# Kernel optimization log

Measured on AMD Instinct MI355X. Metric: run time of the kernel, lower is better.

## Reference

```python
import jax, jax.numpy as jnp
import numpy as np

B_PAIR = 8      # batch_size (identities)
NUM_POS = 4     # images per identity
TEMP = 50.0     # softmax temperature
DIM = 2048
H, W = 24, 12
HALF = B_PAIR * NUM_POS  # 32 samples per modality


def _rand_pairs(rng):
    # mirrors CMAlign._random_pairs
    pos = np.concatenate([rng.permutation(NUM_POS) + NUM_POS * i for i in range(B_PAIR)])
    neg = []
    for i in range(B_PAIR):
        others = np.array([j for j in range(B_PAIR) if j != i])
        bidx = rng.choice(others, NUM_POS, replace=False)
        nidx = rng.permutation(NUM_POS)
        neg.append(bidx * NUM_POS + nidx)
    return pos.astype(np.int32), np.concatenate(neg).astype(np.int32)


def setup_inputs() -> dict:
    key = jax.random.key(0)
    ks = jax.random.split(key, 8)
    feat_v = jax.random.normal(ks[0], (HALF, DIM, H, W), jnp.float32)
    feat_t = jax.random.normal(ks[1], (HALF, DIM, H, W), jnp.float32)
    uncertain_v = jax.random.normal(ks[2], (HALF, 1, H, W), jnp.float32)
    uncertain_t = jax.random.normal(ks[3], (HALF, 1, H, W), jnp.float32)
    q_w = jax.random.normal(ks[4], (DIM // 4, DIM, 3, 3), jnp.float32) * 0.02
    q_b = jnp.zeros((DIM // 4,), jnp.float32)
    k_w = jax.random.normal(ks[5], (DIM // 4, DIM, 3, 3), jnp.float32) * 0.02
    k_b = jnp.zeros((DIM // 4,), jnp.float32)
    rng = np.random.RandomState(0)
    pos_v, neg_v = _rand_pairs(rng)
    pos_t, neg_t = _rand_pairs(rng)
    # visible queries target thermal half (offset), thermal queries target visible half
    pos_idx = jnp.asarray(np.concatenate([pos_v + HALF, pos_t]), jnp.int32)
    neg_idx = jnp.asarray(np.concatenate([neg_v + HALF, neg_t]), jnp.int32)
    return dict(feat_v=feat_v, feat_t=feat_t, uncertain_v=uncertain_v,
                uncertain_t=uncertain_t, q_w=q_w, q_b=q_b, k_w=k_w, k_b=k_b,
                pos_idx=pos_idx, neg_idx=neg_idx)


def _conv3x3(x, w, b):
    y = jax.lax.conv_general_dilated(x, w, window_strides=(1, 1),
                                     padding=((1, 1), (1, 1)),
                                     dimension_numbers=('NCHW', 'OIHW', 'NCHW'))
    return y + b[None, :, None, None]


def _l2n(x, axis):
    # torch F.normalize: x / max(||x||, 1e-12)
    n = jnp.sqrt(jnp.sum(x * x, axis=axis, keepdims=True))
    return x / jnp.maximum(n, 1e-12)


def _cmalign(feat_v, feat_t, q_w, q_b, k_w, k_b, pos_idx, neg_idx):
    feat = jnp.concatenate([feat_v, feat_t], axis=0)  # [B,C,h,w]
    B, C, h, w = feat.shape
    HW = h * w

    # compute_mask (detached): per-sample min-max normalized channel L2 norm
    norms = jnp.sqrt(jnp.sum(feat * feat, axis=1)).reshape(B, HW)
    norms = norms - jnp.min(norms, axis=-1, keepdims=True)
    norms = norms / (jnp.max(norms, axis=-1, keepdims=True) + 1e-12)
    mask = jax.lax.stop_gradient(norms.reshape(B, 1, h, w))

    fq = _conv3x3(feat, q_w, q_b).reshape(B, C // 4, HW)  # query proj shared

    def matching_pr(target):
        fk = _conv3x3(target, k_w, k_b).reshape(B, C // 4, HW)
        sim = jnp.einsum('bcq,bck->bqk', _l2n(fq, 1), _l2n(fk, 1))
        # max-subtract + exp + sum == stable softmax with temperature
        return jax.nn.softmax(TEMP * sim, axis=-1)

    def warp_recon(pr, target):
        warp = jnp.einsum('bqk,bck->bcq', pr, target.reshape(B, C, HW)).reshape(B, C, h, w)
        return mask * warp + (1.0 - mask) * feat

    # positive branch
    tgt_pos = feat[pos_idx]
    pr_pos = matching_pr(tgt_pos)
    mq = mask.reshape(B, HW, 1)
    mk = mask[pos_idx].reshape(B, HW, 1)
    comask = (mq * jnp.einsum('bqk,bko->bqo', pr_pos, mk)).reshape(B, HW)
    comask = comask - jnp.min(comask, axis=-1, keepdims=True)
    comask = comask / (jnp.max(comask, axis=-1, keepdims=True) + 1e-12)
    comask = jax.lax.stop_gradient(comask.reshape(B, h, w))
    feat_recon_pos = warp_recon(pr_pos, tgt_pos)

    # negative branch
    tgt_neg = feat[neg_idx]
    feat_recon_neg = warp_recon(matching_pr(tgt_neg), tgt_neg)

    # triplet margin loss (p=2, margin=0.3, eps=1e-6), distance over channel dim
    d_ap = jnp.sqrt(jnp.sum((feat - feat_recon_pos + 1e-6) ** 2, axis=1))  # [B,h,w]
    d_an = jnp.sqrt(jnp.sum((feat - feat_recon_neg + 1e-6) ** 2, axis=1))
    trip = jnp.maximum(d_ap - d_an + 0.3, 0.0)
    loss = jnp.mean(comask * trip)
    return feat_recon_pos, loss


def reference(feat_v, feat_t, uncertain_v, uncertain_t, q_w, q_b, k_w, k_b, pos_idx, neg_idx):
    # uncertain_v/uncertain_t are concatenated but unused in CMAlign.forward (faithful)
    del uncertain_v, uncertain_t
    return _cmalign(feat_v, feat_t, q_w, q_b, k_w, k_b, pos_idx, neg_idx)
```

## Files before the change

### kernel.cpp

```cpp
#include <hip/hip_runtime.h>
#include <cstdint>
#include <cstddef>


namespace {
constexpr int kB    = 64;
constexpr int kHalf = 32;
constexpr int kC    = 2048;
constexpr int kCQ   = 512;
constexpr int kH    = 24;
constexpr int kW    = 12;
constexpr int kHW   = 288;
constexpr float kTemp = 50.0f;
constexpr int kXPlane = 366;
}

typedef __attribute__((ext_vector_type(8))) __bf16 bf16x8;
typedef __attribute__((ext_vector_type(4))) float f32x4;
typedef __attribute__((ext_vector_type(8))) unsigned short ushort8;

__device__ __forceinline__ const float* feat_base(const float* fv, const float* ft, int b) {
  return (b < kHalf) ? (fv + (size_t)b * kC * kHW)
                     : (ft + (size_t)(b - kHalf) * kC * kHW);
}

__device__ __forceinline__ unsigned short f2bf(float f) {
  union { float f; unsigned u; } c; c.f = f;
  unsigned u = c.u;
  unsigned r = (u + 0x7FFFu + ((u >> 16) & 1u)) >> 16;
  return (unsigned short)r;
}

__device__ __forceinline__ float bf2f(unsigned short h) {
  union { unsigned u; float f; } c; c.u = ((unsigned)h) << 16;
  return c.f;
}

__device__ __forceinline__ void gload_lds16(const void* g, void* l) {
  __builtin_amdgcn_global_load_lds(
      (const __attribute__((address_space(1))) unsigned int*)g,
      (__attribute__((address_space(3))) unsigned int*)l, 16, 0, 0);
}

__global__ void zero_kernel(float* __restrict__ p, int n) {
  int i = blockIdx.x * 256 + threadIdx.x;
  if (i < n) p[i] = 0.f;
}

__global__ __launch_bounds__(256) void prep_w_kernel(const float* __restrict__ qw,
                                                     const float* __restrict__ kw,
                                                     unsigned short* __restrict__ wtq,
                                                     unsigned short* __restrict__ wtk) {
  int oc = blockIdx.x;
  int z  = blockIdx.y;
  const float* w = (z ? kw : qw) + (size_t)oc * (kC * 9);
  unsigned short* wt = z ? wtk : wtq;
  __shared__ unsigned short lw[kC * 9];
  int t = threadIdx.x;
#pragma unroll
  for (int it = 0; it < 18; ++it) {
    int i4 = (it * 256 + t) * 4;
    float4 v = *(const float4*)(w + i4);
    lw[i4 + 0] = f2bf(v.x);
    lw[i4 + 1] = f2bf(v.y);
    lw[i4 + 2] = f2bf(v.z);
    lw[i4 + 3] = f2bf(v.w);
  }
  __syncthreads();
  for (int item = t; item < 9 * 256; item += 256) {
    int tap = item >> 8;
    int icb = item & 255;
    ushort8 pk;
#pragma unroll
    for (int j = 0; j < 8; ++j) pk[j] = lw[(icb * 8 + j) * 9 + tap];
    size_t dst16 = (((size_t)(icb >> 2) * 9 + tap) * 32 + (oc >> 4)) * 64
                   + (oc & 15) + (icb & 3) * 16;
    *(ushort8*)(wt + dst16 * 8) = pk;
  }
}

__global__ __launch_bounds__(512, 1) void conv_fused_kernel(const unsigned short* __restrict__ wtq,
                                                            const unsigned short* __restrict__ wtk,
                                                            const float* __restrict__ qb,
                                                            const float* __restrict__ kb,
                                                            const float* __restrict__ fv,
                                                            const float* __restrict__ ft,
                                                            unsigned short* __restrict__ fqT,
                                                            unsigned short* __restrict__ fkT,
                                                            float* __restrict__ qss,
                                                            float* __restrict__ kss) {
  __shared__ unsigned short Wbuf[2 * 6 * 4096];
  __shared__ unsigned short Xs[4 * kXPlane * 8];
  int t    = threadIdx.x;
  int lane = t & 63;
  int wid  = t >> 6;
  int l15  = lane & 15, kg = lane >> 4;
  int wm   = wid & 1, wn = wid >> 1;
  int n    = blockIdx.x;
  int xcd  = n & 7;
  int oc0  = (xcd >> 1) * 128;
  int b    = ((xcd & 1) << 5) + (n >> 3);
  int f0   = oc0 >> 4;
  const float* fb = feat_base(fv, ft, b);
  const char* wtqB = (const char*)wtq;
  const char* wtkB = (const char*)wtk;

  int  xoff[3];
  bool xvalid[3], xhas[3];
#pragma unroll
  for (int i = 0; i < 3; ++i) {
    int item = i * 512 + t;
    xhas[i] = item < 4 * kXPlane;
    int xkg = item / kXPlane;
    int hp  = item - xkg * kXPlane;
    int hy = hp / 14, hx = hp - hy * 14;
    int y = hy - 1, x = hx - 1;
    bool v = xhas[i] && hp < 364 && (y >= 0 && y < kH && x >= 0 && x < kW);
    xvalid[i] = v;
    xoff[i] = v ? (xkg * 8) * kHW + y * kW + x : 0;
  }

  int aAddr[4];
#pragma unroll
  for (int fm = 0; fm < 4; ++fm)
    aAddr[fm] = (((wm * 4 + fm) * 64) + lane) * 16;
  int nfn = (wn < 2) ? 5 : 4;
  int fnb = (wn < 2) ? wn * 5 : 10 + (wn - 2) * 4;
  int bAddr[5];
#pragma unroll
  for (int fi = 0; fi < 5; ++fi) {
    int p = (fnb + fi) * 16 + l15;
    if (p > 287) p = 287;
    int y = p / kW, x = p - y * kW;
    bAddr[fi] = kg * (kXPlane * 16) + ((y + 1) * 14 + (x + 1)) * 16;
  }

  f32x4 acc[2][4][5];
#pragma unroll
  for (int cv = 0; cv < 2; ++cv)
#pragma unroll
    for (int fm = 0; fm < 4; ++fm)
#pragma unroll
      for (int fi = 0; fi < 5; ++fi) acc[cv][fm][fi] = (f32x4){0.f, 0.f, 0.f, 0.f};

  char* WsB = (char*)Wbuf;
  char* XsB = (char*)Xs;
  int wavebase = t & ~63;

#pragma unroll
  for (int i = 0; i < 3; ++i) {
    if (xhas[i] && !xvalid[i]) {
      ushort8 pk;
#pragma unroll
      for (int j = 0; j < 8; ++j) pk[j] = 0;
      *(ushort8*)(XsB + (size_t)(i * 512 + t) * 16) = pk;
    }
  }
#pragma unroll
  for (int r = 0; r < 3; ++r) {
    size_t g16 = ((size_t)r * 32 + f0 + wid) * 64 + lane;
    gload_lds16(wtqB + g16 * 16, WsB + (size_t)(r * 2 + 0) * 8192 + wavebase * 16);
    gload_lds16(wtkB + g16 * 16, WsB + (size_t)(r * 2 + 1) * 8192 + wavebase * 16);
  }

  int buf = 0;
#pragma unroll 1
  for (int chunk = 0; chunk < 64; ++chunk) {
    int ic0 = chunk * 32;
    {
      float xv[3][8];
#pragma unroll
      for (int i = 0; i < 3; ++i)
        if (xvalid[i]) {
          const float* s = fb + (size_t)ic0 * kHW + xoff[i];
#pragma unroll
          for (int j = 0; j < 8; ++j) xv[i][j] = s[(size_t)j * kHW];
        }
#pragma unroll
      for (int i = 0; i < 3; ++i) {
        if (!xvalid[i]) continue;
        ushort8 pk;
#pragma unroll
        for (int j = 0; j < 8; ++j) pk[j] = f2bf(xv[i][j]);
        *(ushort8*)(XsB + (size_t)(i * 512 + t) * 16) = pk;
      }
    }
    __syncthreads();

#pragma unroll 1
    for (int g = 0; g < 3; ++g) {
      bool hn = (g < 2) || (chunk < 63);
      if (hn) {
        int nchunk = (g < 2) ? chunk : chunk + 1;
        int ng     = (g < 2) ? g + 1 : 0;
#pragma unroll
        for (int r = 0; r < 3; ++r) {
          size_t g16 = ((size_t)(nchunk * 9 + ng * 3 + r) * 32 + f0 + wid) * 64 + lane;
          gload_lds16(wtqB + g16 * 16,
                      WsB + (size_t)((buf ^ 1) * 6 + r * 2 + 0) * 8192 + wavebase * 16);
          gload_lds16(wtkB + g16 * 16,
                      WsB + (size_t)((buf ^ 1) * 6 + r * 2 + 1) * 8192 + wavebase * 16);
        }
      }
#pragma unroll
      for (int r = 0; r < 3; ++r) {
        int tap = g * 3 + r;
        int d16 = ((tap / 3 - 1) * 14 + (tap % 3 - 1)) * 16;
        bf16x8 af[2][4];
#pragma unroll
        for (int cv = 0; cv < 2; ++cv)
#pragma unroll
          for (int fm = 0; fm < 4; ++fm)
            af[cv][fm] = *(const bf16x8*)(WsB + (size_t)(buf * 6 + r * 2 + cv) * 8192 + aAddr[fm]);
#pragma unroll
        for (int fi = 0; fi < 5; ++fi) {
          if (fi >= nfn) continue;
          bf16x8 bb = *(const bf16x8*)(XsB + bAddr[fi] + d16);
#pragma unroll
          for (int cv = 0; cv < 2; ++cv)
#pragma unroll
            for (int fm = 0; fm < 4; ++fm)
              acc[cv][fm][fi] =
                  __builtin_amdgcn_mfma_f32_16x16x32_bf16(af[cv][fm], bb, acc[cv][fm][fi], 0, 0, 0);
        }
      }
      __syncthreads();
      buf ^= 1;
    }
  }

  unsigned short* Ep = Wbuf;
#pragma unroll
  for (int cv = 0; cv < 2; ++cv) {
    const float* bias = cv ? kb : qb;
    float* ssq = cv ? kss : qss;
#pragma unroll
    for (int fi = 0; fi < 5; ++fi) {
      if (fi >= nfn) continue;
      int p = (fnb + fi) * 16 + l15;
      float ps = 0.f;
#pragma unroll
      for (int fm = 0; fm < 4; ++fm)
#pragma unroll
        for (int reg = 0; reg < 4; ++reg) {
          int ocl = wm * 64 + fm * 16 + kg * 4 + reg;
          float v = acc[cv][fm][fi][reg] + bias[oc0 + ocl];
          ps = fmaf(v, v, ps);
          Ep[p * 136 + ocl] = f2bf(v);
        }
      ps += __shfl_xor(ps, 16);
      ps += __shfl_xor(ps, 32);
      if (kg == 0) atomicAdd(ssq + b * kHW + p, ps);
    }
    __syncthreads();
    unsigned short* dstT = (cv ? fkT : fqT) + (size_t)b * kHW * kCQ + oc0;
#pragma unroll
    for (int it = 0; it < 9; ++it) {
      int item = it * 512 + t;
      int p = item >> 4, j = item & 15;
      *(ushort8*)(dstT + (size_t)p * kCQ + j * 8) =
          *(const ushort8*)(Ep + p * 136 + j * 8);
    }
    __syncthreads();
  }
}

__global__ __launch_bounds__(512) void warp_mfma_kernel(const float* __restrict__ fv,
                                                        const float* __restrict__ ft,
                                                        const unsigned short* __restrict__ prb0,
                                                        const unsigned short* __restrict__ prb1,
                                                        const float* __restrict__ maskp,
                                                        const int* __restrict__ pos_idx,
                                                        const int* __restrict__ neg_idx,
                                                        float* __restrict__ outp,
                                                        float* __restrict__ dap,
                                                        float* __restrict__ dan) {
  __shared__ unsigned short AsHi[128 * 32];
  __shared__ unsigned short AsLo[128 * 32];
  __shared__ unsigned short Bs[288 * 32];
  int t    = threadIdx.x;
  int lane = t & 63;
  int wid  = t >> 6;
  int l15  = lane & 15, kg = lane >> 4;
  int wm   = wid >> 1, wn = wid & 1;
  int c0   = blockIdx.x * 128;
  int b    = blockIdx.y;
  int z    = blockIdx.z;
  int write_out = (z == 0);
  const unsigned short* prb = z ? prb1 : prb0;
  float* dsq = z ? dan : dap;
  int tb   = (z ? neg_idx : pos_idx)[b];
  const float* tgt = feat_base(fv, ft, tb);
  const float* fb  = feat_base(fv, ft, b);

  int ar = t >> 2, as = t & 3;
  int aslot = as ^ ((ar ^ (ar >> 2)) & 3);
  unsigned short* aDstHi = AsHi + ar * 32 + aslot * 8;
  unsigned short* aDstLo = AsLo + ar * 32 + aslot * 8;

  int aIdx[2];
#pragma unroll
  for (int fm = 0; fm < 2; ++fm) {
    int r = wm * 32 + fm * 16 + l15;
    aIdx[fm] = r * 32 + (kg ^ ((r ^ (r >> 2)) & 3)) * 8;
  }
  int bIdx[9];
#pragma unroll
  for (int fn = 0; fn < 9; ++fn) {
    int q = wn * 144 + fn * 16 + l15;
    bIdx[fn] = q * 32 + (kg ^ ((q ^ (q >> 2)) & 3)) * 8;
  }

  f32x4 acc[2][9];
#pragma unroll
  for (int fm = 0; fm < 2; ++fm)
#pragma unroll
    for (int fn = 0; fn < 9; ++fn) acc[fm][fn] = (f32x4){0.f, 0.f, 0.f, 0.f};

#pragma unroll 1
  for (int chunk = 0; chunk < 9; ++chunk) {
    int k0 = chunk * 32;
    __syncthreads();
    {
      const float* s = tgt + (size_t)(c0 + ar) * kHW + k0 + as * 8;
      float4 v0 = *(const float4*)(s);
      float4 v1 = *(const float4*)(s + 4);
      float xs[8] = {v0.x, v0.y, v0.z, v0.w, v1.x, v1.y, v1.z, v1.w};
      ushort8 hi, lo;
#pragma unroll
      for (int j = 0; j < 8; ++j) {
        unsigned short h = f2bf(xs[j]);
        hi[j] = h;
        lo[j] = f2bf(xs[j] - bf2f(h));
      }
      *(ushort8*)aDstHi = hi;
      *(ushort8*)aDstLo = lo;
    }
#pragma unroll
    for (int i = 0; i < 3; ++i) {
      int item = i * 512 + t;
      if (item < 1152) {
        int q = item >> 2, s = item & 3;
        ushort8 v = *(const ushort8*)(prb + ((size_t)b * kHW + q) * kHW + k0 + s * 8);
        *(ushort8*)(Bs + q * 32 + (s ^ ((q ^ (q >> 2)) & 3)) * 8) = v;
      }
    }
    __syncthreads();
    bf16x8 ah0 = *(const bf16x8*)(AsHi + aIdx[0]);
    bf16x8 al0 = *(const bf16x8*)(AsLo + aIdx[0]);
    bf16x8 ah1 = *(const bf16x8*)(AsHi + aIdx[1]);
    bf16x8 al1 = *(const bf16x8*)(AsLo + aIdx[1]);
#pragma unroll
    for (int fn = 0; fn < 9; ++fn) {
      bf16x8 bb = *(const bf16x8*)(Bs + bIdx[fn]);
      acc[0][fn] = __builtin_amdgcn_mfma_f32_16x16x32_bf16(ah0, bb, acc[0][fn], 0, 0, 0);
      acc[0][fn] = __builtin_amdgcn_mfma_f32_16x16x32_bf16(al0, bb, acc[0][fn], 0, 0, 0);
      acc[1][fn] = __builtin_amdgcn_mfma_f32_16x16x32_bf16(ah1, bb, acc[1][fn], 0, 0, 0);
      acc[1][fn] = __builtin_amdgcn_mfma_f32_16x16x32_bf16(al1, bb, acc[1][fn], 0, 0, 0);
    }
  }

#pragma unroll
  for (int fn = 0; fn < 9; ++fn) {
    int q = wn * 144 + fn * 16 + l15;
    float mj = maskp[b * kHW + q];
    float psum = 0.f;
#pragma unroll
    for (int fm = 0; fm < 2; ++fm) {
#pragma unroll
      for (int reg = 0; reg < 4; ++reg) {
        int c = c0 + wm * 32 + fm * 16 + kg * 4 + reg;
        float fvv = fb[(size_t)c * kHW + q];
        float Wv  = acc[fm][fn][reg];
        float d   = mj * (fvv - Wv) + 1e-6f;
        psum      = fmaf(d, d, psum);
        if (write_out)
          outp[((size_t)b * kC + c) * kHW + q] = mj * Wv + (1.f - mj) * fvv;
      }
    }
    psum += __shfl_xor(psum, 16);
    psum += __shfl_xor(psum, 32);
    if (lane < 16) atomicAdd(&dsq[b * kHW + q], psum);
  }
}

__global__ __launch_bounds__(320) void mask_part_kernel(const float* __restrict__ fv,
                                                        const float* __restrict__ ft,
                                                        float* __restrict__ part) {
  int b = blockIdx.x;
  int s = blockIdx.y;
  int t = threadIdx.x;
  if (t >= kHW) return;
  const float* fb = feat_base(fv, ft, b) + (size_t)(s * 512) * kHW;
  float sum = 0.f;
  for (int c = 0; c < 512; ++c) { float v = fb[(size_t)c * kHW + t]; sum += v * v; }
  part[((size_t)b * 4 + s) * kHW + t] = sum;
}

__global__ __launch_bounds__(320) void mask_fin_kernel(const float* __restrict__ part,
                                                       float* __restrict__ mask) {
  int b = blockIdx.x;
  int t = threadIdx.x;
  float n = 0.f;
  if (t < kHW) {
    const float* pb = part + (size_t)b * 4 * kHW;
    n = sqrtf(pb[t] + pb[kHW + t] + pb[2 * kHW + t] + pb[3 * kHW + t]);
  }
  __shared__ float sh[320];
  sh[t] = (t < kHW) ? n : 3.4e38f;
  __syncthreads();
  float mn;
  {
    float m = 3.4e38f;
    if (t < 64) {
      for (int i = t; i < 320; i += 64) m = fminf(m, sh[i]);
      for (int off = 32; off; off >>= 1) m = fminf(m, __shfl_xor(m, off));
    }
    __syncthreads();
    if (t == 0) sh[0] = m;
    __syncthreads();
    mn = sh[0];
    __syncthreads();
  }
  sh[t] = (t < kHW) ? n : -3.4e38f;
  __syncthreads();
  float mx;
  {
    float m = -3.4e38f;
    if (t < 64) {
      for (int i = t; i < 320; i += 64) m = fmaxf(m, sh[i]);
      for (int off = 32; off; off >>= 1) m = fmaxf(m, __shfl_xor(m, off));
    }
    __syncthreads();
    if (t == 0) sh[0] = m;
    __syncthreads();
    mx = sh[0];
  }
  if (t < kHW) mask[b * kHW + t] = (n - mn) / ((mx - mn) + 1e-12f);
}

__global__ __launch_bounds__(512, 1) void sim_mfma_kernel(const unsigned short* __restrict__ fqT,
                                                          const unsigned short* __restrict__ fkT,
                                                          const float* __restrict__ qss,
                                                          const float* __restrict__ kss,
                                                          const int* __restrict__ pos_idx,
                                                          const int* __restrict__ neg_idx,
                                                          unsigned short* __restrict__ prb0,
                                                          unsigned short* __restrict__ prb1) {
  __shared__ float Sbuf[96 * 289];
  unsigned short* As = (unsigned short*)Sbuf;
  unsigned short* Bs = (unsigned short*)((char*)Sbuf + 6144);
  float (*S)[289] = (float(*)[289])Sbuf;
  int t    = threadIdx.x;
  int lane = t & 63;
  int wid  = t >> 6;
  int l15  = lane & 15, kg = lane >> 4;
  int wm   = wid & 1, wn = wid >> 1;
  int q0   = blockIdx.x * 96;
  int b    = blockIdx.y;
  int z    = blockIdx.z;
  int tb   = (z ? neg_idx : pos_idx)[b];
  unsigned short* prb = z ? prb1 : prb0;
  const unsigned short* fqb = fqT + ((size_t)b * kHW + q0) * kCQ;
  const unsigned short* fkb = fkT + (size_t)tb * kHW * kCQ;

  int aIdx[3];
#pragma unroll
  for (int fm = 0; fm < 3; ++fm) {
    int r = wm * 48 + fm * 16 + l15;
    aIdx[fm] = r * 32 + (kg ^ ((r ^ (r >> 2)) & 3)) * 8;
  }
  int nfn = (wn < 2) ? 5 : 4;
  int fnb = (wn < 2) ? wn * 5 : 10 + (wn - 2) * 4;
  int bIdx[5];
#pragma unroll
  for (int fi = 0; fi < 5; ++fi) {
    int kr = (fnb + fi) * 16 + l15;
    if (kr > 287) kr = 287;
    bIdx[fi] = kr * 32 + (kg ^ ((kr ^ (kr >> 2)) & 3)) * 8;
  }

  f32x4 acc[3][5];
#pragma unroll
  for (int fm = 0; fm < 3; ++fm)
#pragma unroll
    for (int fi = 0; fi < 5; ++fi) acc[fm][fi] = (f32x4){0.f, 0.f, 0.f, 0.f};

#pragma unroll 1
  for (int chunk = 0; chunk < 16; ++chunk) {
    int c0 = chunk * 32;
    __syncthreads();
    if (t < 384) {
      int ar = t >> 2, as = t & 3;
      ushort8 v = *(const ushort8*)(fqb + (size_t)ar * kCQ + c0 + as * 8);
      int slot = as ^ ((ar ^ (ar >> 2)) & 3);
      *(ushort8*)(As + ar * 32 + slot * 8) = v;
    }
#pragma unroll
    for (int i = 0; i < 3; ++i) {
      int item = i * 512 + t;
      if (item < 1152) {
        int kr = item >> 2, ks = item & 3;
        ushort8 v = *(const ushort8*)(fkb + (size_t)kr * kCQ + c0 + ks * 8);
        int slot = ks ^ ((kr ^ (kr >> 2)) & 3);
        *(ushort8*)(Bs + kr * 32 + slot * 8) = v;
      }
    }
    __syncthreads();
    bf16x8 a[3];
#pragma unroll
    for (int fm = 0; fm < 3; ++fm) a[fm] = *(const bf16x8*)(As + aIdx[fm]);
#pragma unroll
    for (int fi = 0; fi < 5; ++fi) {
      if (fi >= nfn) continue;
      bf16x8 bb = *(const bf16x8*)(Bs + bIdx[fi]);
#pragma unroll
      for (int fm = 0; fm < 3; ++fm)
        acc[fm][fi] = __builtin_amdgcn_mfma_f32_16x16x32_bf16(a[fm], bb, acc[fm][fi], 0, 0, 0);
    }
  }
  __syncthreads();

  float kinvv[5];
#pragma unroll
  for (int fi = 0; fi < 5; ++fi) {
    int col = (fnb + fi) * 16 + l15;
    if (col > 287) col = 287;
    kinvv[fi] = 1.f / fmaxf(sqrtf(kss[tb * kHW + col]), 1e-12f);
  }
#pragma unroll
  for (int fm = 0; fm < 3; ++fm)
#pragma unroll
    for (int reg = 0; reg < 4; ++reg) {
      int row = wm * 48 + fm * 16 + kg * 4 + reg;
      float qi = kTemp / fmaxf(sqrtf(qss[b * kHW + q0 + row]), 1e-12f);
#pragma unroll
      for (int fi = 0; fi < 5; ++fi) {
        if (fi >= nfn) continue;
        S[row][(fnb + fi) * 16 + l15] = qi * kinvv[fi] * acc[fm][fi][reg];
      }
    }
  __syncthreads();

  int l = lane;
  for (int q = wid; q < 96; q += 8) {
    float v[5];
    float m = -3.4e38f;
#pragma unroll
    for (int j = 0; j < 5; ++j) {
      int k = l + 64 * j;
      v[j] = (k < kHW) ? S[q][k] : -3.4e38f;
      m = fmaxf(m, v[j]);
    }
    for (int off = 32; off; off >>= 1) m = fmaxf(m, __shfl_xor(m, off));
    float e[5];
    float s = 0.f;
#pragma unroll
    for (int j = 0; j < 5; ++j) {
      int k = l + 64 * j;
      e[j] = (k < kHW) ? __expf(v[j] - m) : 0.f;
      s += e[j];
    }
    for (int off = 32; off; off >>= 1) s += __shfl_xor(s, off);
    float invs = 1.f / s;
    unsigned short* row = prb + ((size_t)b * kHW + q0 + q) * kHW;
#pragma unroll
    for (int j = 0; j < 5; ++j) {
      int k = l + 64 * j;
      if (k < kHW) row[k] = f2bf(e[j] * invs);
    }
  }
}

__global__ __launch_bounds__(320) void comask_kernel(const unsigned short* __restrict__ prb,
                                                     const float* __restrict__ mask,
                                                     const int* __restrict__ idx,
                                                     float* __restrict__ comask) {
  int b = blockIdx.x;
  int t = threadIdx.x;
  int tb = idx[b];
  __shared__ float mt[kHW];
  __shared__ float cm[kHW];
  __shared__ float red[320];
  if (t < kHW) mt[t] = mask[tb * kHW + t];
  __syncthreads();
  int wv = t >> 6, l = t & 63;
  for (int q = wv; q < kHW; q += 5) {
    const unsigned short* prow = prb + ((size_t)b * kHW + q) * kHW;
    float s = 0.f;
    for (int k = l; k < kHW; k += 64) s += bf2f(prow[k]) * mt[k];
    for (int off = 32; off; off >>= 1) s += __shfl_xor(s, off);
    if (l == 0) cm[q] = mask[b * kHW + q] * s;
  }
  __syncthreads();
  float v = (t < kHW) ? cm[t] : 0.f;
  red[t] = (t < kHW) ? v : 3.4e38f;
  __syncthreads();
  float mn;
  {
    float m = 3.4e38f;
    if (t < 64) {
      for (int i = t; i < 320; i += 64) m = fminf(m, red[i]);
      for (int off = 32; off; off >>= 1) m = fminf(m, __shfl_xor(m, off));
    }
    __syncthreads();
    if (t == 0) red[0] = m;
    __syncthreads();
    mn = red[0];
    __syncthreads();
  }
  red[t] = (t < kHW) ? v : -3.4e38f;
  __syncthreads();
  float mx;
  {
    float m = -3.4e38f;
    if (t < 64) {
      for (int i = t; i < 320; i += 64) m = fmaxf(m, red[i]);
      for (int off = 32; off; off >>= 1) m = fmaxf(m, __shfl_xor(m, off));
    }
    __syncthreads();
    if (t == 0) red[0] = m;
    __syncthreads();
    mx = red[0];
  }
  if (t < kHW) comask[b * kHW + t] = (v - mn) / ((mx - mn) + 1e-12f);
}

__global__ __launch_bounds__(256) void loss_kernel(const float* __restrict__ dap,
                                                   const float* __restrict__ dan,
                                                   const float* __restrict__ comask,
                                                   float* __restrict__ out) {
  int t = threadIdx.x;
  float s = 0.f;
  for (int i = t; i < kB * kHW; i += 256) {
    float da = sqrtf(dap[i]);
    float db = sqrtf(dan[i]);
    float tr = fmaxf(da - db + 0.3f, 0.f);
    s += comask[i] * tr;
  }
  for (int off = 32; off; off >>= 1) s += __shfl_xor(s, off);
  __shared__ float sh[4];
  if ((t & 63) == 0) sh[t >> 6] = s;
  __syncthreads();
  if (t == 0)
    out[(size_t)kB * kC * kHW] = (sh[0] + sh[1] + sh[2] + sh[3]) * (1.f / (float)(kB * kHW));
}

extern "C" void kernel_launch(void* const* d_in, const int* in_sizes, int n_in,
                              void* d_out, int out_size, void* d_ws, size_t ws_size,
                              hipStream_t stream) {
  const float* fv = (const float*)d_in[0];
  const float* ft = (const float*)d_in[1];
  const float* qw = (const float*)d_in[4];
  const float* qb = (const float*)d_in[5];
  const float* kw = (const float*)d_in[6];
  const float* kb = (const float*)d_in[7];
  const int* pos_idx = (const int*)d_in[8];
  const int* neg_idx = (const int*)d_in[9];
  float* out = (float*)d_out;

  constexpr size_t kFQ = (size_t)kB * kCQ * kHW;
  constexpr size_t kPR = (size_t)kB * kHW * kHW;
  float* ws   = (float*)d_ws;
  unsigned short* fqT = (unsigned short*)ws;
  unsigned short* fkT = fqT + (size_t)kB * kHW * kCQ;
  unsigned short* prb0 = (unsigned short*)(ws + kFQ);
  unsigned short* prb1 = prb0 + kPR;
  unsigned short* wtq = (unsigned short*)(ws + 2 * kFQ);
  unsigned short* wtk = wtq + (size_t)9 * kCQ * kC;
  float* part = (float*)wtq;
  float* maskb   = (float*)(wtk + (size_t)9 * kCQ * kC);
  float* qss     = maskb + kB * kHW;
  float* kss     = qss + kB * kHW;
  float* comaskb = kss + kB * kHW;
  float* dap     = comaskb + kB * kHW;
  float* dan     = dap + kB * kHW;
  if (ws_size < (size_t)113688576) return;

  zero_kernel<<<dim3((5 * kB * kHW + 255) / 256), 256, 0, stream>>>(qss, 5 * kB * kHW);
  mask_part_kernel<<<dim3(kB, 4), 320, 0, stream>>>(fv, ft, part);
  mask_fin_kernel<<<dim3(kB), 320, 0, stream>>>(part, maskb);
  prep_w_kernel<<<dim3(kCQ, 2), 256, 0, stream>>>(qw, kw, wtq, wtk);
  conv_fused_kernel<<<dim3(256), 512, 0, stream>>>(wtq, wtk, qb, kb, fv, ft,
                                                   fqT, fkT, qss, kss);

  sim_mfma_kernel<<<dim3(3, kB, 2), 512, 0, stream>>>(fqT, fkT, qss, kss,
                                                      pos_idx, neg_idx, prb0, prb1);
  comask_kernel<<<dim3(kB), 320, 0, stream>>>(prb0, maskb, pos_idx, comaskb);
  warp_mfma_kernel<<<dim3(16, kB, 2), 512, 0, stream>>>(fv, ft, prb0, prb1, maskb,
                                                        pos_idx, neg_idx, out, dap, dan);

  loss_kernel<<<dim3(1), 256, 0, stream>>>(dap, dan, comaskb, out);
}
```

Before: 1.164 ms.

## Fuse mask norm into conv and comask into sim and loss kernels

```diff
diff --git a/kernel.cpp b/kernel.cpp
--- a/kernel.cpp
+++ b/kernel.cpp
@@ -88,7 +88,8 @@
                                                             unsigned short* __restrict__ fqT,
                                                             unsigned short* __restrict__ fkT,
                                                             float* __restrict__ qss,
-                                                            float* __restrict__ kss) {
+                                                            float* __restrict__ kss,
+                                                            float* __restrict__ maskb) {
   __shared__ unsigned short Wbuf[2 * 6 * 4096];
   __shared__ unsigned short Xs[4 * kXPlane * 8];
   int t    = threadIdx.x;
@@ -143,6 +144,8 @@
 #pragma unroll
       for (int fi = 0; fi < 5; ++fi) acc[cv][fm][fi] = (f32x4){0.f, 0.f, 0.f, 0.f};
 
+  float msum0 = 0.f, msum1 = 0.f, msum2 = 0.f;
+
   char* WsB = (char*)Wbuf;
   char* XsB = (char*)Xs;
   int wavebase = t & ~63;
@@ -176,6 +179,18 @@
 #pragma unroll
           for (int j = 0; j < 8; ++j) xv[i][j] = s[(size_t)j * kHW];
         }
+      if (xvalid[0]) {
+#pragma unroll
+        for (int j = 0; j < 8; ++j) msum0 = fmaf(xv[0][j], xv[0][j], msum0);
+      }
+      if (xvalid[1]) {
+#pragma unroll
+        for (int j = 0; j < 8; ++j) msum1 = fmaf(xv[1][j], xv[1][j], msum1);
+      }
+      if (xvalid[2]) {
+#pragma unroll
+        for (int j = 0; j < 8; ++j) msum2 = fmaf(xv[2][j], xv[2][j], msum2);
+      }
 #pragma unroll
       for (int i = 0; i < 3; ++i) {
         if (!xvalid[i]) continue;
@@ -227,6 +242,56 @@
       __syncthreads();
       buf ^= 1;
     }
+  }
+
+  if (oc0 == 0) {
+    float* Mred = (float*)Xs;
+    float msum[3] = {msum0, msum1, msum2};
+#pragma unroll
+    for (int i = 0; i < 3; ++i) {
+      if (!xvalid[i]) continue;
+      int item = i * 512 + t;
+      int xkg = item / kXPlane;
+      int hp  = item - xkg * kXPlane;
+      int y = hp / 14 - 1, x = hp % 14 - 1;
+      Mred[xkg * kHW + y * kW + x] = msum[i];
+    }
+    __syncthreads();
+    float nv = 0.f;
+    if (t < kHW)
+      nv = sqrtf(Mred[t] + Mred[kHW + t] + Mred[2 * kHW + t] + Mred[3 * kHW + t]);
+    float* red = (float*)Wbuf;
+    red[t] = (t < kHW) ? nv : 3.4e38f;
+    __syncthreads();
+    float mn;
+    {
+      float m = 3.4e38f;
+      if (t < 64) {
+        for (int i = t; i < 512; i += 64) m = fminf(m, red[i]);
+        for (int off = 32; off; off >>= 1) m = fminf(m, __shfl_xor(m, off));
+      }
+      __syncthreads();
+      if (t == 0) red[0] = m;
+      __syncthreads();
+      mn = red[0];
+      __syncthreads();
+    }
+    red[t] = (t < kHW) ? nv : -3.4e38f;
+    __syncthreads();
+    float mx;
+    {
+      float m = -3.4e38f;
+      if (t < 64) {
+        for (int i = t; i < 512; i += 64) m = fmaxf(m, red[i]);
+        for (int off = 32; off; off >>= 1) m = fmaxf(m, __shfl_xor(m, off));
+      }
+      __syncthreads();
+      if (t == 0) red[0] = m;
+      __syncthreads();
+      mx = red[0];
+    }
+    if (t < kHW) maskb[b * kHW + t] = (nv - mn) / ((mx - mn) + 1e-12f);
+    __syncthreads();
   }
 
   unsigned short* Ep = Wbuf;
@@ -384,70 +449,18 @@
   }
 }
 
-__global__ __launch_bounds__(320) void mask_part_kernel(const float* __restrict__ fv,
-                                                        const float* __restrict__ ft,
-                                                        float* __restrict__ part) {
-  int b = blockIdx.x;
-  int s = blockIdx.y;
-  int t = threadIdx.x;
-  if (t >= kHW) return;
-  const float* fb = feat_base(fv, ft, b) + (size_t)(s * 512) * kHW;
-  float sum = 0.f;
-  for (int c = 0; c < 512; ++c) { float v = fb[(size_t)c * kHW + t]; sum += v * v; }
-  part[((size_t)b * 4 + s) * kHW + t] = sum;
-}
-
-__global__ __launch_bounds__(320) void mask_fin_kernel(const float* __restrict__ part,
-                                                       float* __restrict__ mask) {
-  int b = blockIdx.x;
-  int t = threadIdx.x;
-  float n = 0.f;
-  if (t < kHW) {
-    const float* pb = part + (size_t)b * 4 * kHW;
-    n = sqrtf(pb[t] + pb[kHW + t] + pb[2 * kHW + t] + pb[3 * kHW + t]);
-  }
-  __shared__ float sh[320];
-  sh[t] = (t < kHW) ? n : 3.4e38f;
-  __syncthreads();
-  float mn;
-  {
-    float m = 3.4e38f;
-    if (t < 64) {
-      for (int i = t; i < 320; i += 64) m = fminf(m, sh[i]);
-      for (int off = 32; off; off >>= 1) m = fminf(m, __shfl_xor(m, off));
-    }
-    __syncthreads();
-    if (t == 0) sh[0] = m;
-    __syncthreads();
-    mn = sh[0];
-    __syncthreads();
-  }
-  sh[t] = (t < kHW) ? n : -3.4e38f;
-  __syncthreads();
-  float mx;
-  {
-    float m = -3.4e38f;
-    if (t < 64) {
-      for (int i = t; i < 320; i += 64) m = fmaxf(m, sh[i]);
-      for (int off = 32; off; off >>= 1) m = fmaxf(m, __shfl_xor(m, off));
-    }
-    __syncthreads();
-    if (t == 0) sh[0] = m;
-    __syncthreads();
-    mx = sh[0];
-  }
-  if (t < kHW) mask[b * kHW + t] = (n - mn) / ((mx - mn) + 1e-12f);
-}
-
 __global__ __launch_bounds__(512, 1) void sim_mfma_kernel(const unsigned short* __restrict__ fqT,
                                                           const unsigned short* __restrict__ fkT,
                                                           const float* __restrict__ qss,
                                                           const float* __restrict__ kss,
+                                                          const float* __restrict__ maskb,
                                                           const int* __restrict__ pos_idx,
                                                           const int* __restrict__ neg_idx,
                                                           unsigned short* __restrict__ prb0,
-                                                          unsigned short* __restrict__ prb1) {
+                                                          unsigned short* __restrict__ prb1,
+                                                          float* __restrict__ craw) {
   __shared__ float Sbuf[96 * 289];
+  __shared__ float mtl[kHW];
   unsigned short* As = (unsigned short*)Sbuf;
   unsigned short* Bs = (unsigned short*)((char*)Sbuf + 6144);
   float (*S)[289] = (float(*)[289])Sbuf;
@@ -464,6 +477,8 @@
   const unsigned short* fqb = fqT + ((size_t)b * kHW + q0) * kCQ;
   const unsigned short* fkb = fkT + (size_t)tb * kHW * kCQ;
 
+  if (t < kHW) mtl[t] = maskb[tb * kHW + t];
+
   int aIdx[3];
 #pragma unroll
   for (int fm = 0; fm < 3; ++fm) {
@@ -564,86 +579,73 @@
     for (int off = 32; off; off >>= 1) s += __shfl_xor(s, off);
     float invs = 1.f / s;
     unsigned short* row = prb + ((size_t)b * kHW + q0 + q) * kHW;
+    float dot = 0.f;
 #pragma unroll
     for (int j = 0; j < 5; ++j) {
       int k = l + 64 * j;
-      if (k < kHW) row[k] = f2bf(e[j] * invs);
-    }
-  }
-}
-
-__global__ __launch_bounds__(320) void comask_kernel(const unsigned short* __restrict__ prb,
-                                                     const float* __restrict__ mask,
-                                                     const int* __restrict__ idx,
-                                                     float* __restrict__ comask) {
-  int b = blockIdx.x;
-  int t = threadIdx.x;
-  int tb = idx[b];
-  __shared__ float mt[kHW];
-  __shared__ float cm[kHW];
-  __shared__ float red[320];
-  if (t < kHW) mt[t] = mask[tb * kHW + t];
-  __syncthreads();
-  int wv = t >> 6, l = t & 63;
-  for (int q = wv; q < kHW; q += 5) {
-    const unsigned short* prow = prb + ((size_t)b * kHW + q) * kHW;
-    float s = 0.f;
-    for (int k = l; k < kHW; k += 64) s += bf2f(prow[k]) * mt[k];
-    for (int off = 32; off; off >>= 1) s += __shfl_xor(s, off);
-    if (l == 0) cm[q] = mask[b * kHW + q] * s;
-  }
-  __syncthreads();
-  float v = (t < kHW) ? cm[t] : 0.f;
-  red[t] = (t < kHW) ? v : 3.4e38f;
-  __syncthreads();
-  float mn;
-  {
-    float m = 3.4e38f;
-    if (t < 64) {
-      for (int i = t; i < 320; i += 64) m = fminf(m, red[i]);
-      for (int off = 32; off; off >>= 1) m = fminf(m, __shfl_xor(m, off));
-    }
-    __syncthreads();
-    if (t == 0) red[0] = m;
-    __syncthreads();
-    mn = red[0];
-    __syncthreads();
-  }
-  red[t] = (t < kHW) ? v : -3.4e38f;
-  __syncthreads();
-  float mx;
-  {
-    float m = -3.4e38f;
-    if (t < 64) {
-      for (int i = t; i < 320; i += 64) m = fmaxf(m, red[i]);
-      for (int off = 32; off; off >>= 1) m = fmaxf(m, __shfl_xor(m, off));
-    }
-    __syncthreads();
-    if (t == 0) red[0] = m;
-    __syncthreads();
-    mx = red[0];
-  }
-  if (t < kHW) comask[b * kHW + t] = (v - mn) / ((mx - mn) + 1e-12f);
+      if (k < kHW) {
+        float p = e[j] * invs;
+        row[k] = f2bf(p);
+        if (z == 0) dot = fmaf(bf2f(f2bf(p)), mtl[k], dot);
+      }
+    }
+    if (z == 0) {
+      for (int off = 32; off; off >>= 1) dot += __shfl_xor(dot, off);
+      if (l == 0)
+        craw[b * kHW + q0 + q] = maskb[b * kHW + q0 + q] * dot;
+    }
+  }
 }
 
 __global__ __launch_bounds__(256) void loss_kernel(const float* __restrict__ dap,
                                                    const float* __restrict__ dan,
-                                                   const float* __restrict__ comask,
+                                                   const float* __restrict__ craw,
                                                    float* __restrict__ out) {
   int t = threadIdx.x;
-  float s = 0.f;
-  for (int i = t; i < kB * kHW; i += 256) {
-    float da = sqrtf(dap[i]);
-    float db = sqrtf(dan[i]);
-    float tr = fmaxf(da - db + 0.3f, 0.f);
-    s += comask[i] * tr;
-  }
-  for (int off = 32; off; off >>= 1) s += __shfl_xor(s, off);
-  __shared__ float sh[4];
-  if ((t & 63) == 0) sh[t >> 6] = s;
+  int wv = t >> 6, l = t & 63;
+  __shared__ float sh4a[4], sh4b[4];
+  __shared__ float sh2[2];
+  float total = 0.f;
+#pragma unroll 1
+  for (int b = 0; b < kB; ++b) {
+    const float* cb = craw + b * kHW;
+    float v1 = cb[t];
+    float v2 = (t < kHW - 256) ? cb[t + 256] : v1;
+    float mnl = fminf(v1, v2), mxl = fmaxf(v1, v2);
+    for (int off = 32; off; off >>= 1) {
+      mnl = fminf(mnl, __shfl_xor(mnl, off));
+      mxl = fmaxf(mxl, __shfl_xor(mxl, off));
+    }
+    if (l == 0) { sh4a[wv] = mnl; sh4b[wv] = mxl; }
+    __syncthreads();
+    if (t == 0) {
+      float mn = sh4a[0], mx = sh4b[0];
+      for (int i = 1; i < 4; ++i) { mn = fminf(mn, sh4a[i]); mx = fmaxf(mx, sh4b[i]); }
+      sh2[0] = mn; sh2[1] = mx;
+    }
+    __syncthreads();
+    float mn = sh2[0];
+    float inv = 1.f / ((sh2[1] - mn) + 1e-12f);
+    {
+      int i = b * kHW + t;
+      float cn = (v1 - mn) * inv;
+      float tr = fmaxf(sqrtf(dap[i]) - sqrtf(dan[i]) + 0.3f, 0.f);
+      total = fmaf(cn, tr, total);
+    }
+    if (t < kHW - 256) {
+      int i = b * kHW + t + 256;
+      float cn = (v2 - mn) * inv;
+      float tr = fmaxf(sqrtf(dap[i]) - sqrtf(dan[i]) + 0.3f, 0.f);
+      total = fmaf(cn, tr, total);
+    }
+    __syncthreads();
+  }
+  for (int off = 32; off; off >>= 1) total += __shfl_xor(total, off);
+  if (l == 0) sh4a[wv] = total;
   __syncthreads();
   if (t == 0)
-    out[(size_t)kB * kC * kHW] = (sh[0] + sh[1] + sh[2] + sh[3]) * (1.f / (float)(kB * kHW));
+    out[(size_t)kB * kC * kHW] =
+        (sh4a[0] + sh4a[1] + sh4a[2] + sh4a[3]) * (1.f / (float)(kB * kHW));
 }
 
 extern "C" void kernel_launch(void* const* d_in, const int* in_sizes, int n_in,
@@ -668,27 +670,21 @@
   unsigned short* prb1 = prb0 + kPR;
   unsigned short* wtq = (unsigned short*)(ws + 2 * kFQ);
   unsigned short* wtk = wtq + (size_t)9 * kCQ * kC;
-  float* part = (float*)wtq;
   float* maskb   = (float*)(wtk + (size_t)9 * kCQ * kC);
   float* qss     = maskb + kB * kHW;
   float* kss     = qss + kB * kHW;
-  float* comaskb = kss + kB * kHW;
-  float* dap     = comaskb + kB * kHW;
+  float* craw    = kss + kB * kHW;
+  float* dap     = craw + kB * kHW;
   float* dan     = dap + kB * kHW;
   if (ws_size < (size_t)113688576) return;
 
   zero_kernel<<<dim3((5 * kB * kHW + 255) / 256), 256, 0, stream>>>(qss, 5 * kB * kHW);
-  mask_part_kernel<<<dim3(kB, 4), 320, 0, stream>>>(fv, ft, part);
-  mask_fin_kernel<<<dim3(kB), 320, 0, stream>>>(part, maskb);
   prep_w_kernel<<<dim3(kCQ, 2), 256, 0, stream>>>(qw, kw, wtq, wtk);
   conv_fused_kernel<<<dim3(256), 512, 0, stream>>>(wtq, wtk, qb, kb, fv, ft,
-                                                   fqT, fkT, qss, kss);
-
-  sim_mfma_kernel<<<dim3(3, kB, 2), 512, 0, stream>>>(fqT, fkT, qss, kss,
-                                                      pos_idx, neg_idx, prb0, prb1);
-  comask_kernel<<<dim3(kB), 320, 0, stream>>>(prb0, maskb, pos_idx, comaskb);
+                                                   fqT, fkT, qss, kss, maskb);
+  sim_mfma_kernel<<<dim3(3, kB, 2), 512, 0, stream>>>(fqT, fkT, qss, kss, maskb,
+                                                      pos_idx, neg_idx, prb0, prb1, craw);
   warp_mfma_kernel<<<dim3(16, kB, 2), 512, 0, stream>>>(fv, ft, prb0, prb1, maskb,
                                                         pos_idx, neg_idx, out, dap, dan);
-
-  loss_kernel<<<dim3(1), 256, 0, stream>>>(dap, dan, comaskb, out);
-}
+  loss_kernel<<<dim3(1), 256, 0, stream>>>(dap, dan, craw, out);
+}
```

Result: no change. 1.144 ms (-1.7%).
